# Kernel optimization log

Measured on AMD Instinct MI355X. Metric: run time of the kernel, lower is better.

The kernel has to match this reference:

```python
import jax, jax.numpy as jnp
import numpy as np

R = 1024          # number of 'a' tokens merged per sample
PROTECT_CLS = True


def setup_inputs() -> dict:
    key = jax.random.key(0)
    k1, k2 = jax.random.split(key)
    B, T, C = 8, 4096, 512
    x = jax.random.normal(k1, (B, T, C), dtype=jnp.float32)
    k = jax.random.normal(k2, (B, T, C), dtype=jnp.float32)
    return {"x": x, "k": k}


def reference(x, k):
    B, T, C = x.shape
    r = R
    pos_a = jnp.arange(0, T, 2)          # (Ta,)
    pos_b = jnp.arange(1, T, 2)          # (Tb,)
    Tb = pos_b.shape[0]

    # cosine-similarity scores between even ('a') and odd ('b') keys
    a = k[:, ::2, :]
    b = k[:, 1::2, :]
    a = a / (jnp.linalg.norm(a, axis=-1, keepdims=True) + 1e-12)
    b = b / (jnp.linalg.norm(b, axis=-1, keepdims=True) + 1e-12)
    scores = jnp.einsum('bac,bdc->bad', a, b)   # (B, Ta, Tb)
    if PROTECT_CLS:
        scores = scores.at[:, 0, :].set(-jnp.inf)

    node_max = jnp.max(scores, axis=-1)          # (B, Ta)
    node_idx = jnp.argmax(scores, axis=-1)       # (B, Ta) best 'b' partner per 'a'
    edge_order = jnp.argsort(-node_max, axis=-1) # descending
    src_idx = edge_order[:, :r]                  # merged 'a' tokens
    unm_sorted = jnp.sort(edge_order[:, r:], axis=-1)  # unmerged 'a', sorted
    dst_idx = jnp.take_along_axis(node_idx, src_idx, axis=-1)  # (B, r)

    src_tok = x[:, ::2, :]
    dst_tok = x[:, 1::2, :]
    unm = jnp.take_along_axis(src_tok, unm_sorted[..., None], axis=1)      # (B, Ta-r, C)
    src_sel = jnp.take_along_axis(src_tok, src_idx[..., None], axis=1)     # (B, r, C)
    dst_updated = jax.vmap(lambda d, i, s: d.at[i].add(s))(dst_tok, dst_idx, src_sel)
    merged = jnp.concatenate([unm, dst_updated], axis=1)                   # (B, Ta-r+Tb, C)

    base_b = unm.shape[1]
    unm_pos = pos_a[unm_sorted]   # (B, Ta-r) original positions of unmerged 'a'
    src_pos = pos_a[src_idx]      # (B, r)    original positions of merged 'a'

    def build_si(up, sp, di):
        si = jnp.full((T,), -1, dtype=jnp.int32)
        si = si.at[up].set(jnp.arange(base_b, dtype=jnp.int32))
        si = si.at[pos_b].set(base_b + jnp.arange(Tb, dtype=jnp.int32))
        si = si.at[sp].set((base_b + di).astype(jnp.int32))
        return si

    source_index = jax.vmap(build_si)(unm_pos, src_pos, dst_idx)  # (B, T)
    return merged, source_index
```

## Files before the change

kernel.cpp:

```cpp
#include <hip/hip_runtime.h>
#include <stdint.h>

#define BN 8
#define TN 4096
#define CN 512
#define TA 2048
#define RR 1024
#define BASEB 1024
#define MROWS 3072
#define KC 64
#define NCHUNK (CN / KC)
#define CAP 64
#define DCAP 32

typedef _Float16 f16x8 __attribute__((ext_vector_type(8)));
typedef float f32x4 __attribute__((ext_vector_type(4)));
typedef __attribute__((address_space(3))) uint32_t lds_u32_t;
typedef __attribute__((address_space(1))) const uint32_t g_u32_t;

__device__ __forceinline__ unsigned ofloat(float f) {
    unsigned u = __float_as_uint(f);
    return (u & 0x80000000u) ? ~u : (u | 0x80000000u);
}
__device__ __forceinline__ float unofloat(unsigned u) {
    unsigned v = (u & 0x80000000u) ? (u ^ 0x80000000u) : ~u;
    return __uint_as_float(v);
}

__global__ __launch_bounds__(256) void split_kernel(const float* __restrict__ k,
        _Float16* __restrict__ Ahi, _Float16* __restrict__ Bhi,
        float* __restrict__ invA, float* __restrict__ invB,
        float* __restrict__ nHa, float* __restrict__ nLa,
        float* __restrict__ Pq, float* __restrict__ Qq,
        unsigned long long* __restrict__ nodekey,
        int* __restrict__ cnt, unsigned* __restrict__ maxHH,
        int* __restrict__ dcnt) {
    int row = blockIdx.x * 4 + (threadIdx.x >> 6);
    int lane = threadIdx.x & 63;
    const float* p = k + (size_t)row * CN;
    float4 v1 = *(const float4*)(p + lane * 8);
    float4 v2 = *(const float4*)(p + lane * 8 + 4);
    float s = v1.x*v1.x + v1.y*v1.y + v1.z*v1.z + v1.w*v1.w
            + v2.x*v2.x + v2.y*v2.y + v2.z*v2.z + v2.w*v2.w;
    #pragma unroll
    for (int off = 32; off > 0; off >>= 1) s += __shfl_xor(s, off);
    float inv = 1.0f / (sqrtf(s) + 1e-12f);
    float sc = 1024.0f * inv;
    float m[8] = {v1.x*sc, v1.y*sc, v1.z*sc, v1.w*sc,
                  v2.x*sc, v2.y*sc, v2.z*sc, v2.w*sc};
    f16x8 H;
    float h2 = 0.f, l2 = 0.f;
    #pragma unroll
    for (int jj = 0; jj < 8; ++jj) {
        _Float16 h = (_Float16)m[jj];
        H[jj] = h;
        float hf = (float)h;
        float lf = m[jj] - hf;
        h2 += hf * hf;
        l2 += lf * lf;
    }
    #pragma unroll
    for (int off = 32; off > 0; off >>= 1) {
        h2 += __shfl_xor(h2, off);
        l2 += __shfl_xor(l2, off);
    }
    float nh = sqrtf(h2), nl = sqrtf(l2);
    int b = row >> 12;
    int tt = row & 4095;
    int node = tt >> 1;
    size_t dst = (((size_t)(b * NCHUNK + (lane >> 3)) * TA + node)) * KC
               + (lane & 7) * 8;
    if (tt & 1) {
        *(f16x8*)(Bhi + dst) = H;
        if (lane == 0) {
            invB[b * TA + node] = inv;
            Pq[b * TA + node] = nl + 1.2f + 4e-5f * nh;
            Qq[b * TA + node] = nh + nl + 1050.0f;
            nodekey[b * TA + node] =
                (((unsigned long long)0x007FFFFFu) << 32) | 0xFFFFFFFFull;
            cnt[b * TA + node] = 0;
            maxHH[b * TA + node] = 0u;
            dcnt[b * TA + node] = 0;
        }
    } else {
        *(f16x8*)(Ahi + dst) = H;
        if (lane == 0) {
            invA[b * TA + node] = inv;
            nHa[b * TA + node] = nh;
            nLa[b * TA + node] = nl;
        }
    }
}

__global__ __launch_bounds__(256, 4) void score_hh_kernel(
        const _Float16* __restrict__ Ahi, const _Float16* __restrict__ Bhi,
        const float* __restrict__ nHa, const float* __restrict__ nLa,
        const float* __restrict__ Pq, const float* __restrict__ Qq,
        int* __restrict__ cnt, unsigned* __restrict__ maxHH,
        int* __restrict__ candJ, float* __restrict__ candS) {
    __shared__ _Float16 lds[2 * 128 * KC];
    __shared__ float rowmax2[128][2];
    const int lid = blockIdx.x;
    const int b  = lid & 7;
    const int t  = lid >> 3;
    const int i0 = (t & 15) << 7;
    const int j0 = (t >> 4) << 7;
    const int tid = threadIdx.x;
    const int lane = tid & 63;
    const int w = tid >> 6;
    const int wr = (w >> 1) * 64;
    const int wc = (w & 1) * 64;

    const size_t chunkstride = (size_t)TA * KC;
    const size_t batchbase = (size_t)b * NCHUNK * chunkstride;
    const _Float16* pbase[2] = { Ahi + batchbase + (size_t)i0 * KC,
                                 Bhi + batchbase + (size_t)j0 * KC };
    int srcoff[8];
    #pragma unroll
    for (int i = 0; i < 8; ++i) {
        int s = (i & 3) * 256 + tid;
        int n = s >> 3, sg = s & 7;
        srcoff[i] = n * KC + ((sg ^ (n & 7)) * 8);
    }

    f32x4 acc[4][4];
    #pragma unroll
    for (int m = 0; m < 4; ++m)
        #pragma unroll
        for (int n = 0; n < 4; ++n) acc[m][n] = (f32x4){0.f, 0.f, 0.f, 0.f};

    const int fr = lane & 15, ks = lane >> 4;
    int rowbaseA[4], rowbaseB[4];
    #pragma unroll
    for (int m = 0; m < 4; ++m) rowbaseA[m] = (wr + m * 16 + fr) * KC;
    #pragma unroll
    for (int n = 0; n < 4; ++n) rowbaseB[n] = (wc + n * 16 + fr) * KC;

    for (int kt = 0; kt < NCHUNK; ++kt) {
        const size_t cb = (size_t)kt * chunkstride;
        #pragma unroll
        for (int i = 0; i < 8; ++i) {
            _Float16* lp = lds + (i >> 2) * 8192 + ((i & 3) * 256 + tid) * 8;
            __builtin_amdgcn_global_load_lds(
                (g_u32_t*)(pbase[i >> 2] + cb + srcoff[i]),
                (lds_u32_t*)lp, 16, 0, 0);
        }
        __syncthreads();
        #pragma unroll
        for (int kk = 0; kk < 2; ++kk) {
            const int slo = (((kk << 2) + ks) ^ (fr & 7)) * 8;
            f16x8 bh[4];
            #pragma unroll
            for (int n = 0; n < 4; ++n)
                bh[n] = *(const f16x8*)(&lds[8192 + rowbaseB[n] + slo]);
            #pragma unroll
            for (int m = 0; m < 4; ++m) {
                f16x8 ah = *(const f16x8*)(&lds[rowbaseA[m] + slo]);
                #pragma unroll
                for (int n = 0; n < 4; ++n)
                    acc[m][n] = __builtin_amdgcn_mfma_f32_16x16x32_f16(ah, bh[n], acc[m][n], 0, 0, 0);
            }
        }
        __syncthreads();
    }

    float wmax[4][4];
    #pragma unroll
    for (int m = 0; m < 4; ++m)
        #pragma unroll
        for (int reg = 0; reg < 4; ++reg) {
            float mx = acc[m][0][reg];
            #pragma unroll
            for (int n = 1; n < 4; ++n) mx = fmaxf(mx, acc[m][n][reg]);
            #pragma unroll
            for (int mm2 = 8; mm2 > 0; mm2 >>= 1)
                mx = fmaxf(mx, __shfl_xor(mx, mm2, 16));
            wmax[m][reg] = mx;
        }
    if (fr == 0) {
        #pragma unroll
        for (int m = 0; m < 4; ++m)
            #pragma unroll
            for (int reg = 0; reg < 4; ++reg) {
                int r = wr + m * 16 + ks * 4 + reg;
                rowmax2[r][w & 1] = wmax[m][reg];
            }
    }
    __syncthreads();
    if (fr == 0) {
        #pragma unroll
        for (int m = 0; m < 4; ++m)
            #pragma unroll
            for (int reg = 0; reg < 4; ++reg) {
                int r = wr + m * 16 + ks * 4 + reg;
                atomicMax(&maxHH[b * TA + i0 + r], ofloat(wmax[m][reg]));
            }
    }
    float Pj[4], Qj[4];
    #pragma unroll
    for (int n = 0; n < 4; ++n) {
        int j = j0 + wc + n * 16 + fr;
        Pj[n] = Pq[b * TA + j];
        Qj[n] = Qq[b * TA + j];
    }
    #pragma unroll
    for (int m = 0; m < 4; ++m)
        #pragma unroll
        for (int reg = 0; reg < 4; ++reg) {
            int r = wr + m * 16 + ks * 4 + reg;
            int i = i0 + r;
            float M = fmaxf(rowmax2[r][0], rowmax2[r][1]);
            float ha = nHa[b * TA + i], la = nLa[b * TA + i];
            #pragma unroll
            for (int n = 0; n < 4; ++n) {
                float s = acc[m][n][reg];
                if (s >= M - (ha * Pj[n] + la * Qj[n])) {
                    int j = j0 + wc + n * 16 + fr;
                    int idx = atomicAdd(&cnt[b * TA + i], 1);
                    if (idx < CAP) {
                        candJ[(size_t)(b * TA + i) * CAP + idx] = j;
                        candS[(size_t)(b * TA + i) * CAP + idx] = s;
                    }
                }
            }
        }
}

__global__ __launch_bounds__(256) void rescore_kernel(const float* __restrict__ k,
        const float* __restrict__ invA, const float* __restrict__ invB,
        const float* __restrict__ nHa, const float* __restrict__ nLa,
        const float* __restrict__ Pq, const float* __restrict__ Qq,
        const int* __restrict__ cnt, const unsigned* __restrict__ maxHH,
        const int* __restrict__ candJ, const float* __restrict__ candS,
        unsigned long long* __restrict__ nodekey) {
    const int b = blockIdx.y;
    const int wv = threadIdx.x >> 6;
    const int lane = threadIdx.x & 63;
    const int i = blockIdx.x * 4 + wv;
    if (i == 0) return;
    const size_t base = (size_t)b * TA;
    float inva = invA[base + i];
    const float* ka = k + ((size_t)b * TN + 2 * i) * CN + lane * 8;
    float a[8];
    #pragma unroll
    for (int e = 0; e < 8; ++e) a[e] = ka[e] * inva;
    int c_n = cnt[base + i];
    float gmax = unofloat(maxHH[base + i]);
    float ha = nHa[base + i], la = nLa[base + i];
    unsigned bhi = 0u, blo = 0u;

    if (c_n <= CAP) {
        for (int c = 0; c < c_n; ++c) {
            int j = candJ[(base + i) * CAP + c];
            float s = candS[(base + i) * CAP + c];
            if (s < gmax - (ha * Pq[base + j] + la * Qq[base + j])) continue;
            float invb = invB[base + j];
            const float* kb = k + ((size_t)b * TN + 2 * j + 1) * CN + lane * 8;
            float d = 0.f;
            #pragma unroll
            for (int e = 0; e < 8; ++e) d += a[e] * (kb[e] * invb);
            #pragma unroll
            for (int off = 32; off > 0; off >>= 1) d += __shfl_xor(d, off);
            unsigned khi = ofloat(d), klo = 0xFFFFFFFFu - (unsigned)j;
            if (khi > bhi || (khi == bhi && klo > blo)) { bhi = khi; blo = klo; }
        }
    } else {
        for (int j = 0; j < TA; ++j) {
            float invb = invB[base + j];
            const float* kb = k + ((size_t)b * TN + 2 * j + 1) * CN + lane * 8;
            float d = 0.f;
            #pragma unroll
            for (int e = 0; e < 8; ++e) d += a[e] * (kb[e] * invb);
            #pragma unroll
            for (int off = 32; off > 0; off >>= 1) d += __shfl_xor(d, off);
            unsigned khi = ofloat(d), klo = 0xFFFFFFFFu - (unsigned)j;
            if (khi > bhi || (khi == bhi && klo > blo)) { bhi = khi; blo = klo; }
        }
    }
    if (lane == 0)
        nodekey[base + i] = (((unsigned long long)bhi) << 32) | blo;
}

__global__ __launch_bounds__(256) void rank_flag_kernel(
        const unsigned long long* __restrict__ nodekey,
        int* __restrict__ is_src) {
    __shared__ unsigned long long K[2048];
    const int b = blockIdx.y;
    const int t = threadIdx.x;
    for (int i = t; i < 2048; i += 256) {
        unsigned hi = (unsigned)(nodekey[b * TA + i] >> 32);
        K[i] = (((unsigned long long)hi) << 32) | (unsigned)(2047 - i);
    }
    __syncthreads();
    const int i = blockIdx.x * 256 + t;
    const unsigned long long ki = K[i];
    int rank = 0;
    #pragma unroll 8
    for (int j = 0; j < 2048; ++j) rank += (K[j] > ki) ? 1 : 0;
    is_src[b * TA + i] = (rank < RR) ? 1 : 0;
}

__global__ __launch_bounds__(1024) void scan_si_kernel(const int* __restrict__ is_src,
        const unsigned long long* __restrict__ nodekey,
        float* __restrict__ out_si, int* __restrict__ rank2node,
        int* __restrict__ dcnt, int* __restrict__ dlist,
        int* __restrict__ aidx) {
    __shared__ int ps[2048];
    __shared__ unsigned char fl[2048];
    const int b = blockIdx.x;
    const int t = threadIdx.x;
    int s0 = is_src[b * TA + t];
    int s1 = is_src[b * TA + 1024 + t];
    int f0 = 1 - s0, f1 = 1 - s1;
    fl[t] = (unsigned char)s0;
    fl[t + 1024] = (unsigned char)s1;
    ps[t] = f0;
    ps[t + 1024] = f1;
    __syncthreads();
    for (int off = 1; off < 2048; off <<= 1) {
        int v0 = (t >= off) ? ps[t - off] : 0;
        int v1 = ((t + 1024) >= off) ? ps[t + 1024 - off] : 0;
        __syncthreads();
        ps[t] += v0;
        ps[t + 1024] += v1;
        __syncthreads();
    }
    int u0 = ps[t] - f0, u1 = ps[t + 1024] - f1;
    #pragma unroll
    for (int h = 0; h < 2; ++h) {
        int i = t + h * 1024;
        int u = h ? u1 : u0;
        int val;
        if (fl[i]) {
            unsigned j = 0xFFFFFFFFu - (unsigned)(nodekey[b * TA + i] & 0xFFFFFFFFull);
            val = BASEB + (int)j;
            int idx = atomicAdd(&dcnt[b * TA + (int)j], 1);
            aidx[b * TA + i] = idx;
            if (idx < DCAP)
                dlist[((size_t)b * TA + (int)j) * DCAP + idx] = i;
        } else {
            val = u;
            rank2node[b * BASEB + u] = i;
        }
        out_si[(size_t)b * TN + 2 * i]     = (float)val;
        out_si[(size_t)b * TN + 2 * i + 1] = (float)(BASEB + i);
    }
}

__global__ __launch_bounds__(128) void move_kernel(const float* __restrict__ x,
        const int* __restrict__ rank2node, const int* __restrict__ dcnt,
        const int* __restrict__ dlist, float* __restrict__ out) {
    const int b = blockIdx.y;
    const int r = blockIdx.x;
    float4* dst = (float4*)(out + ((size_t)b * MROWS + r) * CN);
    if (r < BASEB) {
        int i = rank2node[b * BASEB + r];
        const float4* src = (const float4*)(x + ((size_t)b * TN + 2 * i) * CN);
        dst[threadIdx.x] = src[threadIdx.x];
    } else {
        int j = r - BASEB;
        const float4* sd = (const float4*)(x + ((size_t)b * TN + 2 * j + 1) * CN);
        float4 v = sd[threadIdx.x];
        int c = dcnt[b * TA + j];
        if (c > DCAP) c = DCAP;
        for (int s = 0; s < c; ++s) {
            int i = dlist[((size_t)b * TA + j) * DCAP + s];
            const float4* ss = (const float4*)(x + ((size_t)b * TN + 2 * i) * CN);
            float4 w = ss[threadIdx.x];
            v.x += w.x; v.y += w.y; v.z += w.z; v.w += w.w;
        }
        dst[threadIdx.x] = v;
    }
}

__global__ __launch_bounds__(256) void overflow_kernel(const float* __restrict__ x,
        const int* __restrict__ is_src, const int* __restrict__ aidx,
        const unsigned long long* __restrict__ nodekey,
        float* __restrict__ out) {
    const int b = blockIdx.y;
    const int i = blockIdx.x * 256 + threadIdx.x;
    if (!is_src[b * TA + i] || aidx[b * TA + i] < DCAP) return;
    unsigned j = 0xFFFFFFFFu - (unsigned)(nodekey[b * TA + i] & 0xFFFFFFFFull);
    const float* src = x + ((size_t)b * TN + 2 * i) * CN;
    float* dst = out + ((size_t)b * MROWS + BASEB + j) * CN;
    for (int c = 0; c < CN; ++c) atomicAdd(&dst[c], src[c]);
}

extern "C" void kernel_launch(void* const* d_in, const int* in_sizes, int n_in,
                              void* d_out, int out_size, void* d_ws, size_t ws_size,
                              hipStream_t stream) {
    const float* x = (const float*)d_in[0];
    const float* k = (const float*)d_in[1];
    float* out = (float*)d_out;
    float* out_si = out + (size_t)BN * MROWS * CN;

    char* ws = (char*)d_ws;
    const size_t PLANE = (size_t)BN * TA * CN;
    _Float16* Ahi = (_Float16*)ws;
    _Float16* Bhi = Ahi + PLANE;
    char* tail = ws + 2 * PLANE * sizeof(_Float16);
    const size_t NN = (size_t)BN * TA;
    float* invA = (float*)(tail);
    float* invB = invA + NN;
    float* nHa  = invB + NN;
    float* nLa  = nHa + NN;
    float* Pq   = nLa + NN;
    float* Qq   = Pq + NN;
    unsigned long long* nodekey = (unsigned long long*)(Qq + NN);
    int* cnt        = (int*)(nodekey + NN);
    unsigned* maxHH = (unsigned*)(cnt + NN);
    int* is_src     = (int*)(maxHH + NN);
    int* dcnt       = is_src + NN;
    int* aidx       = dcnt + NN;
    int* rank2node  = aidx + NN;
    int* candJ      = rank2node + (size_t)BN * BASEB;
    float* candS    = (float*)(candJ + NN * CAP);
    int* dlist      = (int*)(candS + NN * CAP);

    split_kernel<<<dim3(BN * TN / 4), dim3(256), 0, stream>>>(
        k, Ahi, Bhi, invA, invB, nHa, nLa, Pq, Qq, nodekey, cnt, maxHH, dcnt);
    score_hh_kernel<<<dim3(2048), dim3(256), 0, stream>>>(
        Ahi, Bhi, nHa, nLa, Pq, Qq, cnt, maxHH, candJ, candS);
    rescore_kernel<<<dim3(512, BN), dim3(256), 0, stream>>>(
        k, invA, invB, nHa, nLa, Pq, Qq, cnt, maxHH, candJ, candS, nodekey);
    rank_flag_kernel<<<dim3(8, BN), dim3(256), 0, stream>>>(nodekey, is_src);
    scan_si_kernel<<<dim3(BN), dim3(1024), 0, stream>>>(
        is_src, nodekey, out_si, rank2node, dcnt, dlist, aidx);
    move_kernel<<<dim3(MROWS, BN), dim3(128), 0, stream>>>(
        x, rank2node, dcnt, dlist, out);
    overflow_kernel<<<dim3(TA / 256, BN), dim3(256), 0, stream>>>(
        x, is_src, aidx, nodekey, out);
}
```

Baseline: 182.2 us.

## Stage full-depth B tile in LDS and stream A fragments from global

The score GEMM now loads a 64-column B tile across the full channel depth into LDS once, then each wave reads its A fragments directly from global memory, with no per-chunk LDS staging or barriers. Tiles shrink to 128x64 and the grid doubles. Each wave now owns whole rows of the tile, so the per-row max is taken within one wave and the cross-wave shared rowmax reduction goes away. Candidates are thresholded against this tile-local max, so more of them may pass, and CAP rises from 64 to 96 to hold them. The trade-off is 64KB of LDS per block, lower occupancy (launch bounds 2), and uncached global A loads sitting in the MFMA loop.

New measurement: 299.3 us. 64.2% more time.

```diff
diff --git a/kernel.cpp b/kernel.cpp
--- a/kernel.cpp
+++ b/kernel.cpp
@@ -10,7 +10,7 @@
 #define MROWS 3072
 #define KC 64
 #define NCHUNK (CN / KC)
-#define CAP 64
+#define CAP 96
 #define DCAP 32
 
 typedef _Float16 f16x8 __attribute__((ext_vector_type(8)));
@@ -92,130 +92,103 @@
     }
 }
 
-__global__ __launch_bounds__(256, 4) void score_hh_kernel(
+__global__ __launch_bounds__(256, 2) void score_bstat_kernel(
         const _Float16* __restrict__ Ahi, const _Float16* __restrict__ Bhi,
         const float* __restrict__ nHa, const float* __restrict__ nLa,
         const float* __restrict__ Pq, const float* __restrict__ Qq,
         int* __restrict__ cnt, unsigned* __restrict__ maxHH,
         int* __restrict__ candJ, float* __restrict__ candS) {
-    __shared__ _Float16 lds[2 * 128 * KC];
-    __shared__ float rowmax2[128][2];
+    __shared__ _Float16 ldsB[64 * CN];
     const int lid = blockIdx.x;
     const int b  = lid & 7;
     const int t  = lid >> 3;
     const int i0 = (t & 15) << 7;
-    const int j0 = (t >> 4) << 7;
+    const int j0 = (t >> 4) << 6;
     const int tid = threadIdx.x;
     const int lane = tid & 63;
     const int w = tid >> 6;
-    const int wr = (w >> 1) * 64;
-    const int wc = (w & 1) * 64;
 
     const size_t chunkstride = (size_t)TA * KC;
     const size_t batchbase = (size_t)b * NCHUNK * chunkstride;
-    const _Float16* pbase[2] = { Ahi + batchbase + (size_t)i0 * KC,
-                                 Bhi + batchbase + (size_t)j0 * KC };
-    int srcoff[8];
-    #pragma unroll
-    for (int i = 0; i < 8; ++i) {
-        int s = (i & 3) * 256 + tid;
-        int n = s >> 3, sg = s & 7;
-        srcoff[i] = n * KC + ((sg ^ (n & 7)) * 8);
-    }
-
-    f32x4 acc[4][4];
-    #pragma unroll
-    for (int m = 0; m < 4; ++m)
+
+    #pragma unroll
+    for (int it = 0; it < 16; ++it) {
+        int s = it * 256 + tid;
+        int node = s >> 6;
+        int w6 = s & 63;
+        int kc = w6 >> 3, sl = w6 & 7;
+        const _Float16* gp = Bhi + batchbase + (size_t)kc * chunkstride
+            + (size_t)(j0 + node) * KC + ((sl ^ (node & 7)) * 8);
+        __builtin_amdgcn_global_load_lds((g_u32_t*)gp,
+            (lds_u32_t*)(ldsB + s * 8), 16, 0, 0);
+    }
+    __syncthreads();
+
+    const int fr = lane & 15, ks = lane >> 4;
+    f32x4 acc[2][4];
+    #pragma unroll
+    for (int m = 0; m < 2; ++m)
         #pragma unroll
         for (int n = 0; n < 4; ++n) acc[m][n] = (f32x4){0.f, 0.f, 0.f, 0.f};
 
-    const int fr = lane & 15, ks = lane >> 4;
-    int rowbaseA[4], rowbaseB[4];
-    #pragma unroll
-    for (int m = 0; m < 4; ++m) rowbaseA[m] = (wr + m * 16 + fr) * KC;
-    #pragma unroll
-    for (int n = 0; n < 4; ++n) rowbaseB[n] = (wc + n * 16 + fr) * KC;
-
-    for (int kt = 0; kt < NCHUNK; ++kt) {
-        const size_t cb = (size_t)kt * chunkstride;
+    const _Float16* aBase = Ahi + batchbase
+        + (size_t)(i0 + w * 32 + fr) * KC + ks * 8;
+    int bq[4][2];
+    #pragma unroll
+    for (int n = 0; n < 4; ++n) {
+        int nb = n * 16 + fr;
         #pragma unroll
-        for (int i = 0; i < 8; ++i) {
-            _Float16* lp = lds + (i >> 2) * 8192 + ((i & 3) * 256 + tid) * 8;
-            __builtin_amdgcn_global_load_lds(
-                (g_u32_t*)(pbase[i >> 2] + cb + srcoff[i]),
-                (lds_u32_t*)lp, 16, 0, 0);
-        }
-        __syncthreads();
+        for (int kk = 0; kk < 2; ++kk)
+            bq[n][kk] = nb * CN + ((((kk << 2) + ks) ^ (nb & 7)) * 8);
+    }
+
+    #pragma unroll 2
+    for (int kc = 0; kc < NCHUNK; ++kc) {
+        f16x8 a[2][2];
         #pragma unroll
-        for (int kk = 0; kk < 2; ++kk) {
-            const int slo = (((kk << 2) + ks) ^ (fr & 7)) * 8;
-            f16x8 bh[4];
-            #pragma unroll
-            for (int n = 0; n < 4; ++n)
-                bh[n] = *(const f16x8*)(&lds[8192 + rowbaseB[n] + slo]);
-            #pragma unroll
-            for (int m = 0; m < 4; ++m) {
-                f16x8 ah = *(const f16x8*)(&lds[rowbaseA[m] + slo]);
+        for (int m = 0; m < 2; ++m)
+            #pragma unroll
+            for (int kk = 0; kk < 2; ++kk)
+                a[m][kk] = *(const f16x8*)(aBase + (size_t)kc * chunkstride
+                                           + m * (16 * KC) + kk * 32);
+        #pragma unroll
+        for (int kk = 0; kk < 2; ++kk)
+            #pragma unroll
+            for (int n = 0; n < 4; ++n) {
+                f16x8 bh = *(const f16x8*)(&ldsB[bq[n][kk] + kc * KC]);
                 #pragma unroll
-                for (int n = 0; n < 4; ++n)
-                    acc[m][n] = __builtin_amdgcn_mfma_f32_16x16x32_f16(ah, bh[n], acc[m][n], 0, 0, 0);
+                for (int m = 0; m < 2; ++m)
+                    acc[m][n] = __builtin_amdgcn_mfma_f32_16x16x32_f16(
+                        a[m][kk], bh, acc[m][n], 0, 0, 0);
             }
-        }
-        __syncthreads();
-    }
-
-    float wmax[4][4];
-    #pragma unroll
-    for (int m = 0; m < 4; ++m)
+    }
+
+    float Pj[4], Qj[4];
+    #pragma unroll
+    for (int n = 0; n < 4; ++n) {
+        int j = j0 + n * 16 + fr;
+        Pj[n] = Pq[b * TA + j];
+        Qj[n] = Qq[b * TA + j];
+    }
+    #pragma unroll
+    for (int m = 0; m < 2; ++m)
         #pragma unroll
         for (int reg = 0; reg < 4; ++reg) {
-            float mx = acc[m][0][reg];
-            #pragma unroll
-            for (int n = 1; n < 4; ++n) mx = fmaxf(mx, acc[m][n][reg]);
+            float M = acc[m][0][reg];
+            #pragma unroll
+            for (int n = 1; n < 4; ++n) M = fmaxf(M, acc[m][n][reg]);
             #pragma unroll
             for (int mm2 = 8; mm2 > 0; mm2 >>= 1)
-                mx = fmaxf(mx, __shfl_xor(mx, mm2, 16));
-            wmax[m][reg] = mx;
-        }
-    if (fr == 0) {
-        #pragma unroll
-        for (int m = 0; m < 4; ++m)
-            #pragma unroll
-            for (int reg = 0; reg < 4; ++reg) {
-                int r = wr + m * 16 + ks * 4 + reg;
-                rowmax2[r][w & 1] = wmax[m][reg];
-            }
-    }
-    __syncthreads();
-    if (fr == 0) {
-        #pragma unroll
-        for (int m = 0; m < 4; ++m)
-            #pragma unroll
-            for (int reg = 0; reg < 4; ++reg) {
-                int r = wr + m * 16 + ks * 4 + reg;
-                atomicMax(&maxHH[b * TA + i0 + r], ofloat(wmax[m][reg]));
-            }
-    }
-    float Pj[4], Qj[4];
-    #pragma unroll
-    for (int n = 0; n < 4; ++n) {
-        int j = j0 + wc + n * 16 + fr;
-        Pj[n] = Pq[b * TA + j];
-        Qj[n] = Qq[b * TA + j];
-    }
-    #pragma unroll
-    for (int m = 0; m < 4; ++m)
-        #pragma unroll
-        for (int reg = 0; reg < 4; ++reg) {
-            int r = wr + m * 16 + ks * 4 + reg;
-            int i = i0 + r;
-            float M = fmaxf(rowmax2[r][0], rowmax2[r][1]);
+                M = fmaxf(M, __shfl_xor(M, mm2, 16));
+            int i = i0 + w * 32 + m * 16 + ks * 4 + reg;
+            if (fr == 0)
+                atomicMax(&maxHH[b * TA + i], ofloat(M));
             float ha = nHa[b * TA + i], la = nLa[b * TA + i];
             #pragma unroll
             for (int n = 0; n < 4; ++n) {
                 float s = acc[m][n][reg];
                 if (s >= M - (ha * Pj[n] + la * Qj[n])) {
-                    int j = j0 + wc + n * 16 + fr;
+                    int j = j0 + n * 16 + fr;
                     int idx = atomicAdd(&cnt[b * TA + i], 1);
                     if (idx < CAP) {
                         candJ[(size_t)(b * TA + i) * CAP + idx] = j;
@@ -419,7 +392,7 @@
 
     split_kernel<<<dim3(BN * TN / 4), dim3(256), 0, stream>>>(
         k, Ahi, Bhi, invA, invB, nHa, nLa, Pq, Qq, nodekey, cnt, maxHH, dcnt);
-    score_hh_kernel<<<dim3(2048), dim3(256), 0, stream>>>(
+    score_bstat_kernel<<<dim3(4096), dim3(256), 0, stream>>>(
         Ahi, Bhi, nHa, nLa, Pq, Qq, cnt, maxHH, candJ, candS);
     rescore_kernel<<<dim3(512, BN), dim3(256), 0, stream>>>(
         k, invA, invB, nHa, nLa, Pq, Qq, cnt, maxHH, candJ, candS, nodekey);
```

## Double-buffer LDS K-chunks in score GEMM with smaller chunk size

Applied to the files above, without the earlier changes.

Halves the K chunk from 64 to 32 columns, re-laying out the f16 key buffers and the LDS swizzle to match. Adds two LDS stages so the async global-to-LDS load of the next chunk runs while MFMAs consume the current one, leaving one barrier per iteration instead of two. This aims to hide global load latency in the similarity GEMM. The cost is twice as many loop iterations, each with less compute to cover the load, and a changed swizzle pattern.

Measured after the change: 183.7 us. Within noise of the previous version (+0.8%).

```diff
diff --git a/kernel.cpp b/kernel.cpp
--- a/kernel.cpp
+++ b/kernel.cpp
@@ -8,7 +8,7 @@
 #define RR 1024
 #define BASEB 1024
 #define MROWS 3072
-#define KC 64
+#define KC 32
 #define NCHUNK (CN / KC)
 #define CAP 64
 #define DCAP 32
@@ -68,8 +68,8 @@
     int b = row >> 12;
     int tt = row & 4095;
     int node = tt >> 1;
-    size_t dst = (((size_t)(b * NCHUNK + (lane >> 3)) * TA + node)) * KC
-               + (lane & 7) * 8;
+    size_t dst = (((size_t)(b * NCHUNK + (lane >> 2)) * TA + node)) * KC
+               + (lane & 3) * 8;
     if (tt & 1) {
         *(f16x8*)(Bhi + dst) = H;
         if (lane == 0) {
@@ -98,7 +98,7 @@
         const float* __restrict__ Pq, const float* __restrict__ Qq,
         int* __restrict__ cnt, unsigned* __restrict__ maxHH,
         int* __restrict__ candJ, float* __restrict__ candS) {
-    __shared__ _Float16 lds[2 * 128 * KC];
+    __shared__ _Float16 lds[2 * 2 * 128 * KC];
     __shared__ float rowmax2[128][2];
     const int lid = blockIdx.x;
     const int b  = lid & 7;
@@ -113,14 +113,15 @@
 
     const size_t chunkstride = (size_t)TA * KC;
     const size_t batchbase = (size_t)b * NCHUNK * chunkstride;
-    const _Float16* pbase[2] = { Ahi + batchbase + (size_t)i0 * KC,
-                                 Bhi + batchbase + (size_t)j0 * KC };
-    int srcoff[8];
-    #pragma unroll
-    for (int i = 0; i < 8; ++i) {
-        int s = (i & 3) * 256 + tid;
-        int n = s >> 3, sg = s & 7;
-        srcoff[i] = n * KC + ((sg ^ (n & 7)) * 8);
+    const _Float16* gptr[4];
+    #pragma unroll
+    for (int i = 0; i < 4; ++i) {
+        int s = (i & 1) * 256 + tid;
+        int n = s >> 2, sg = s & 3;
+        int srcoff = n * KC + ((sg ^ ((n >> 1) & 3)) * 8);
+        const _Float16* base = (i < 2) ? Ahi : Bhi;
+        int r0 = (i < 2) ? i0 : j0;
+        gptr[i] = base + batchbase + (size_t)r0 * KC + srcoff;
     }
 
     f32x4 acc[4][4];
@@ -130,39 +131,50 @@
         for (int n = 0; n < 4; ++n) acc[m][n] = (f32x4){0.f, 0.f, 0.f, 0.f};
 
     const int fr = lane & 15, ks = lane >> 4;
-    int rowbaseA[4], rowbaseB[4];
-    #pragma unroll
-    for (int m = 0; m < 4; ++m) rowbaseA[m] = (wr + m * 16 + fr) * KC;
-    #pragma unroll
-    for (int n = 0; n < 4; ++n) rowbaseB[n] = (wc + n * 16 + fr) * KC;
-
+    int aoff[4], boff2[4];
+    #pragma unroll
+    for (int m = 0; m < 4; ++m) {
+        int r = wr + m * 16 + fr;
+        aoff[m] = r * KC + (ks ^ ((r >> 1) & 3)) * 8;
+    }
+    #pragma unroll
+    for (int n = 0; n < 4; ++n) {
+        int r = wc + n * 16 + fr;
+        boff2[n] = r * KC + (ks ^ ((r >> 1) & 3)) * 8;
+    }
+
+    #define STAGE(q, kt)                                                       \
+        _Pragma("unroll")                                                      \
+        for (int i = 0; i < 4; ++i) {                                          \
+            _Float16* lp = lds + (q) * 8192 + i * 2048 + w * 512;              \
+            __builtin_amdgcn_global_load_lds(                                  \
+                (g_u32_t*)(gptr[i] + (size_t)(kt) * chunkstride),              \
+                (lds_u32_t*)lp, 16, 0, 0);                                     \
+        }
+
+    STAGE(0, 0)
+    __syncthreads();
+    #pragma unroll 2
     for (int kt = 0; kt < NCHUNK; ++kt) {
-        const size_t cb = (size_t)kt * chunkstride;
-        #pragma unroll
-        for (int i = 0; i < 8; ++i) {
-            _Float16* lp = lds + (i >> 2) * 8192 + ((i & 3) * 256 + tid) * 8;
-            __builtin_amdgcn_global_load_lds(
-                (g_u32_t*)(pbase[i >> 2] + cb + srcoff[i]),
-                (lds_u32_t*)lp, 16, 0, 0);
+        const int cur = kt & 1;
+        if (kt + 1 < NCHUNK) {
+            STAGE(cur ^ 1, kt + 1)
+        }
+        const _Float16* lb = lds + cur * 8192;
+        f16x8 bh[4];
+        #pragma unroll
+        for (int n = 0; n < 4; ++n)
+            bh[n] = *(const f16x8*)(&lb[4096 + boff2[n]]);
+        #pragma unroll
+        for (int m = 0; m < 4; ++m) {
+            f16x8 ah = *(const f16x8*)(&lb[aoff[m]]);
+            #pragma unroll
+            for (int n = 0; n < 4; ++n)
+                acc[m][n] = __builtin_amdgcn_mfma_f32_16x16x32_f16(ah, bh[n], acc[m][n], 0, 0, 0);
         }
         __syncthreads();
-        #pragma unroll
-        for (int kk = 0; kk < 2; ++kk) {
-            const int slo = (((kk << 2) + ks) ^ (fr & 7)) * 8;
-            f16x8 bh[4];
-            #pragma unroll
-            for (int n = 0; n < 4; ++n)
-                bh[n] = *(const f16x8*)(&lds[8192 + rowbaseB[n] + slo]);
-            #pragma unroll
-            for (int m = 0; m < 4; ++m) {
-                f16x8 ah = *(const f16x8*)(&lds[rowbaseA[m] + slo]);
-                #pragma unroll
-                for (int n = 0; n < 4; ++n)
-                    acc[m][n] = __builtin_amdgcn_mfma_f32_16x16x32_f16(ah, bh[n], acc[m][n], 0, 0, 0);
-            }
-        }
-        __syncthreads();
-    }
+    }
+    #undef STAGE
 
     float wmax[4][4];
     #pragma unroll
```
